# Performance work log

Measured on AMD Instinct MI355X. Metric: run time of the kernel, lower is better.

Reference implementation:

```python
import jax, jax.numpy as jnp
import numpy as np

N, E = 32768, 8192            # num_nodes, num_hyperedges
ND, ED, HD, OD, NH = 128, 128, 64, 128, 4  # node/edge/hidden/output dims, heads
EPS = 1e-8


def min_max_normalize(x):
    # per-feature (column-wise) min-max normalization, as in utils.min_max_normalize_cuda
    mn = x.min(axis=0)
    mx = x.max(axis=0)
    return (x - mn) / (mx - mn + EPS)


def setup_inputs() -> dict:
    key = jax.random.key(0)
    ks = jax.random.split(key, 12)
    s = 0.05
    node_features = jax.random.normal(ks[0], (N, ND), jnp.float32)
    # sparse-ish binary incidence matrix stored dense (as the torch code uses dense mm)
    incidence_matrix = (jax.random.uniform(ks[1], (N, E)) < 0.01).astype(jnp.float32)
    edge_features = jax.random.normal(ks[2], (E, ED), jnp.float32)
    # stacked per-head parameters (heads are chained, so head input dim == ND == OD)
    nodeW = jax.random.normal(ks[3], (NH, ND, HD), jnp.float32) * s
    nodeB = jnp.zeros((NH, HD), jnp.float32)
    edgeW = jax.random.normal(ks[4], (NH, ED, HD), jnp.float32) * s
    edgeB = jnp.zeros((NH, HD), jnp.float32)
    attnW = jax.random.normal(ks[5], (NH, HD, 1), jnp.float32) * s
    attnB = jnp.zeros((NH, 1), jnp.float32)
    outW = jax.random.normal(ks[6], (NH, HD, OD), jnp.float32) * s
    outB = jnp.zeros((NH, OD), jnp.float32)
    return dict(node_features=node_features, incidence_matrix=incidence_matrix,
                edge_features=edge_features, nodeW=nodeW, nodeB=nodeB,
                edgeW=edgeW, edgeB=edgeB, attnW=attnW, attnB=attnB,
                outW=outW, outB=outB)


def reference(node_features, incidence_matrix, edge_features,
              nodeW, nodeB, edgeW, edgeB, attnW, attnB, outW, outB):
    # node degree normalizer, shared across heads
    deg = incidence_matrix.sum(axis=1, keepdims=True) + EPS  # [N, 1]
    x = node_features
    for h in range(NH):  # heads are applied sequentially (chained), per original forward
        tn = x @ nodeW[h] + nodeB[h]                       # [N, HD]
        te = edge_features @ edgeW[h] + edgeB[h]           # [E, HD]
        agg = (incidence_matrix @ te) / deg                # [N, HD] mean over incident edges
        scores = (tn + agg) @ attnW[h] + attnB[h]          # [N, 1]
        scores = jnp.where(scores >= 0, scores, 0.2 * scores)  # LeakyReLU(0.2)
        coeffs = jax.nn.sigmoid(scores)                    # [N, 1]
        upd = coeffs * agg + tn                            # gated residual
        upd = upd @ outW[h] + outB[h]                      # [N, OD]
        upd = min_max_normalize(upd)
        x = jax.nn.relu(upd)                               # ReLU applied after each head
    # dropout is identity at inference; output_transform is defined but never used
    return x
```

## Files before the change

### kernel.cpp

```cpp
#include <hip/hip_runtime.h>
#include <cstdint>
#include <cstddef>

#define N_NODES 32768
#define N_EDGES 8192
#define ND 128
#define HD 64
#define OD 128
#define NH 4
#define EPSV 1e-8f
#define NBLOCKS 256
#define ROWS 128
#define LDW 132

__device__ __forceinline__ unsigned encf(float f) {
  unsigned b = __float_as_uint(f);
  return (b & 0x80000000u) ? ~b : (b | 0x80000000u);
}
__device__ __forceinline__ float decf(unsigned u) {
  unsigned b = (u & 0x80000000u) ? (u & 0x7fffffffu) : ~u;
  return __uint_as_float(b);
}
__device__ __forceinline__ unsigned aload(const unsigned* p) {
  return __hip_atomic_load(p, __ATOMIC_RELAXED, __HIP_MEMORY_SCOPE_AGENT);
}

__device__ __forceinline__ void gsync(unsigned* cnt, unsigned* gen) {
  __syncthreads();
  if (threadIdx.x == 0) {
    __threadfence();
    const unsigned g = __hip_atomic_load(gen, __ATOMIC_ACQUIRE, __HIP_MEMORY_SCOPE_AGENT);
    if (__hip_atomic_fetch_add(cnt, 1u, __ATOMIC_ACQ_REL, __HIP_MEMORY_SCOPE_AGENT) == NBLOCKS - 1u) {
      __hip_atomic_store(cnt, 0u, __ATOMIC_RELAXED, __HIP_MEMORY_SCOPE_AGENT);
      __hip_atomic_store(gen, g + 1u, __ATOMIC_RELEASE, __HIP_MEMORY_SCOPE_AGENT);
    } else {
      while (__hip_atomic_load(gen, __ATOMIC_ACQUIRE, __HIP_MEMORY_SCOPE_AGENT) == g) {
        __builtin_amdgcn_s_sleep(2);
      }
    }
    __threadfence();
  }
  __syncthreads();
}

__global__ __launch_bounds__(512, 2) void k_fused(
    const float* __restrict__ nf, const float* __restrict__ inc,
    const float* __restrict__ ef,
    const float* __restrict__ nodeW, const float* __restrict__ nodeB,
    const float* __restrict__ edgeW, const float* __restrict__ edgeB,
    const float* __restrict__ attnW, const float* __restrict__ attnB,
    const float* __restrict__ outW, const float* __restrict__ outB,
    unsigned* __restrict__ fin_mn, unsigned* __restrict__ fin_mx,
    unsigned* __restrict__ bar_cnt, unsigned* __restrict__ bar_gen,
    float* __restrict__ outp)
{
  __shared__ __align__(16) float xs[ROWS * LDW];
  __shared__ __align__(16) float ps[ROWS * LDW];
  __shared__ float s_deg[ROWS];
  __shared__ int s_idx[2][512];
  __shared__ int s_cnt[2];
  __shared__ float s_red[4 * 128];
  __shared__ float s_mm[8 * 128];

  const int t = threadIdx.x;
  const int r0 = blockIdx.x * ROWS;

  #pragma unroll
  for (int i = 0; i < 8; i++) {
    const int f = t + i * 512;
    const int row = f >> 5;
    const int c4 = (f & 31) * 4;
    *(float4*)&xs[row * LDW + c4] = *(const float4*)(nf + (size_t)(r0 + row) * ND + c4);
  }

  const int dim = t & 127;
  const int sub = t >> 7;
  float4 vreg[4];
  {
    const float* irow = inc + (size_t)r0 * N_EDGES;
    #pragma unroll
    for (int i = 0; i < 4; i++) vreg[i] = *(const float4*)(irow + (t + i * 512) * 4);
  }
  #pragma unroll 1
  for (int row = 0; row < ROWS; row++) {
    const int buf = row & 1;
    if (t == 0) s_cnt[buf] = 0;
    __syncthreads();
    #pragma unroll
    for (int i = 0; i < 4; i++) {
      const int c = (t + i * 512) * 4;
      const float4 v = vreg[i];
      if (v.x != 0.f) s_idx[buf][atomicAdd(&s_cnt[buf], 1)] = c;
      if (v.y != 0.f) s_idx[buf][atomicAdd(&s_cnt[buf], 1)] = c + 1;
      if (v.z != 0.f) s_idx[buf][atomicAdd(&s_cnt[buf], 1)] = c + 2;
      if (v.w != 0.f) s_idx[buf][atomicAdd(&s_cnt[buf], 1)] = c + 3;
    }
    if (row + 1 < ROWS) {
      const float* irow = inc + (size_t)(r0 + row + 1) * N_EDGES;
      #pragma unroll
      for (int i = 0; i < 4; i++) vreg[i] = *(const float4*)(irow + (t + i * 512) * 4);
    }
    __syncthreads();
    const int cnt = min(s_cnt[buf], 512);
    float acc = 0.f;
    int i = sub;
    for (; i + 28 < cnt; i += 32) {
      float sv = 0.f;
      #pragma unroll
      for (int u2 = 0; u2 < 8; u2++) sv += ef[(size_t)s_idx[buf][i + u2 * 4] * ND + dim];
      acc += sv;
    }
    for (; i + 12 < cnt; i += 16) {
      float sv = 0.f;
      #pragma unroll
      for (int u2 = 0; u2 < 4; u2++) sv += ef[(size_t)s_idx[buf][i + u2 * 4] * ND + dim];
      acc += sv;
    }
    for (; i < cnt; i += 4) acc += ef[(size_t)s_idx[buf][i] * ND + dim];
    s_red[sub * 128 + dim] = acc;
    __syncthreads();
    if (t < 128) {
      ps[row * LDW + t] = s_red[t] + s_red[128 + t] + s_red[256 + t] + s_red[384 + t];
      if (t == 0) s_deg[row] = (float)cnt;
    }
  }
  __syncthreads();

  const int lane = t & 63;
  const int wv = t >> 6;
  const int o = lane & 7;
  const int rA = (wv << 4) + (lane >> 3);
  const int rB = rA + 8;
  const int j0 = o * 8;
  const int obase = lane & 56;

  #pragma unroll 1
  for (int h = 0; h < NH; h++) {
    const float* nW = nodeW + (size_t)h * ND * HD;
    const float* eW = edgeW + (size_t)h * ND * HD;
    const float* oW = outW + (size_t)h * HD * OD;
    const float* nB = nodeB + (size_t)h * HD;
    const float* eB = edgeB + (size_t)h * HD;
    const float* aW = attnW + (size_t)h * HD;
    const float  aB = attnB[h];

    if (h > 0) {
      const unsigned* pmn = fin_mn + (size_t)(h - 1) * 128;
      const unsigned* pmx = fin_mx + (size_t)(h - 1) * 128;
      if (t < 128) s_red[t] = decf(aload(&pmn[t]));
      else if (t < 256) s_red[t] = decf(aload(&pmx[t - 128]));
      __syncthreads();
      const int rr = t >> 2;
      const int c0 = (t & 3) * 32;
      #pragma unroll
      for (int i = 0; i < 32; i++) {
        const float mnv = s_red[c0 + i];
        const float mxv = s_red[128 + c0 + i];
        const float v = (xs[rr * LDW + c0 + i] - mnv) / (mxv - mnv + EPSV);
        xs[rr * LDW + c0 + i] = v > 0.f ? v : 0.f;
      }
      __syncthreads();
    }

    float tnA[8], tnB[8], agA[8], agB[8];
    #pragma unroll
    for (int j = 0; j < 8; j++) { tnA[j] = 0.f; tnB[j] = 0.f; agA[j] = 0.f; agB[j] = 0.f; }
    for (int k4 = 0; k4 < ND; k4 += 4) {
      const float4 xa = *(const float4*)&xs[rA * LDW + k4];
      const float4 xb = *(const float4*)&xs[rB * LDW + k4];
      const float4 pa = *(const float4*)&ps[rA * LDW + k4];
      const float4 pb = *(const float4*)&ps[rB * LDW + k4];
      const float xav[4] = {xa.x, xa.y, xa.z, xa.w};
      const float xbv[4] = {xb.x, xb.y, xb.z, xb.w};
      const float pav[4] = {pa.x, pa.y, pa.z, pa.w};
      const float pbv[4] = {pb.x, pb.y, pb.z, pb.w};
      #pragma unroll
      for (int kk = 0; kk < 4; kk++) {
        const int k = k4 + kk;
        const float4 n0 = *(const float4*)(nW + (size_t)k * HD + j0);
        const float4 n1 = *(const float4*)(nW + (size_t)k * HD + j0 + 4);
        const float4 e0 = *(const float4*)(eW + (size_t)k * HD + j0);
        const float4 e1 = *(const float4*)(eW + (size_t)k * HD + j0 + 4);
        const float nn[8] = {n0.x, n0.y, n0.z, n0.w, n1.x, n1.y, n1.z, n1.w};
        const float ee[8] = {e0.x, e0.y, e0.z, e0.w, e1.x, e1.y, e1.z, e1.w};
        #pragma unroll
        for (int j = 0; j < 8; j++) {
          tnA[j] = fmaf(xav[kk], nn[j], tnA[j]);
          tnB[j] = fmaf(xbv[kk], nn[j], tnB[j]);
          agA[j] = fmaf(pav[kk], ee[j], agA[j]);
          agB[j] = fmaf(pbv[kk], ee[j], agB[j]);
        }
      }
    }

    const float rsA = s_deg[rA], rsB = s_deg[rB];
    const float dA = rsA + EPSV, dB = rsB + EPSV;
    const float iA = 1.f / dA, iB = 1.f / dB;
    float spA = 0.f, spB = 0.f;
    #pragma unroll
    for (int j = 0; j < 8; j++) {
      const float nb = nB[j0 + j], eb = eB[j0 + j], aw = aW[j0 + j];
      const float tA = tnA[j] + nb, tB = tnB[j] + nb;
      const float aA = fmaf(rsA, eb, agA[j]) * iA;
      const float aB = fmaf(rsB, eb, agB[j]) * iB;
      tnA[j] = tA; tnB[j] = tB; agA[j] = aA; agB[j] = aB;
      spA = fmaf(tA + aA, aw, spA);
      spB = fmaf(tB + aB, aw, spB);
    }
    spA += __shfl_xor(spA, 1); spA += __shfl_xor(spA, 2); spA += __shfl_xor(spA, 4);
    spB += __shfl_xor(spB, 1); spB += __shfl_xor(spB, 2); spB += __shfl_xor(spB, 4);
    float sA = spA + aB, sB = spB + aB;
    sA = (sA >= 0.f) ? sA : 0.2f * sA;
    sB = (sB >= 0.f) ? sB : 0.2f * sB;
    const float cA = 1.f / (1.f + expf(-sA));
    const float cB = 1.f / (1.f + expf(-sB));
    float uA[8], uB[8];
    #pragma unroll
    for (int j = 0; j < 8; j++) {
      uA[j] = fmaf(cA, agA[j], tnA[j]);
      uB[j] = fmaf(cB, agB[j], tnB[j]);
    }

    const int oc0 = o * 16;
    float ya[16], yb[16];
    #pragma unroll
    for (int i4 = 0; i4 < 4; i4++) {
      const float4 bv = *(const float4*)(outB + (size_t)h * OD + oc0 + i4 * 4);
      ya[i4 * 4 + 0] = bv.x; ya[i4 * 4 + 1] = bv.y; ya[i4 * 4 + 2] = bv.z; ya[i4 * 4 + 3] = bv.w;
      yb[i4 * 4 + 0] = bv.x; yb[i4 * 4 + 1] = bv.y; yb[i4 * 4 + 2] = bv.z; yb[i4 * 4 + 3] = bv.w;
    }
    #pragma unroll 8
    for (int k = 0; k < HD; k++) {
      const float ukA = __shfl(uA[k & 7], obase + (k >> 3));
      const float ukB = __shfl(uB[k & 7], obase + (k >> 3));
      #pragma unroll
      for (int i4 = 0; i4 < 4; i4++) {
        const float4 ov = *(const float4*)(oW + (size_t)k * OD + oc0 + i4 * 4);
        const float oo[4] = {ov.x, ov.y, ov.z, ov.w};
        #pragma unroll
        for (int c = 0; c < 4; c++) {
          ya[i4 * 4 + c] = fmaf(ukA, oo[c], ya[i4 * 4 + c]);
          yb[i4 * 4 + c] = fmaf(ukB, oo[c], yb[i4 * 4 + c]);
        }
      }
    }

    __syncthreads();
    #pragma unroll
    for (int i4 = 0; i4 < 4; i4++) {
      *(float4*)&xs[rA * LDW + oc0 + i4 * 4] =
          make_float4(ya[i4 * 4 + 0], ya[i4 * 4 + 1], ya[i4 * 4 + 2], ya[i4 * 4 + 3]);
      *(float4*)&xs[rB * LDW + oc0 + i4 * 4] =
          make_float4(yb[i4 * 4 + 0], yb[i4 * 4 + 1], yb[i4 * 4 + 2], yb[i4 * 4 + 3]);
    }
    __syncthreads();
    {
      const int col = t & 127;
      const int s4 = t >> 7;
      float lo = 3.4e38f, hi = -3.4e38f;
      for (int r = s4; r < ROWS; r += 4) {
        const float v = xs[r * LDW + col];
        lo = fminf(lo, v); hi = fmaxf(hi, v);
      }
      s_mm[s4 * 128 + col] = lo;
      s_mm[512 + s4 * 128 + col] = hi;
      __syncthreads();
      if (t < 128) {
        const float l = fminf(fminf(s_mm[t], s_mm[128 + t]), fminf(s_mm[256 + t], s_mm[384 + t]));
        const float hh = fmaxf(fmaxf(s_mm[512 + t], s_mm[640 + t]), fmaxf(s_mm[768 + t], s_mm[896 + t]));
        atomicMin(&fin_mn[(size_t)h * 128 + t], encf(l));
        atomicMax(&fin_mx[(size_t)h * 128 + t], encf(hh));
      }
    }
    gsync(bar_cnt, bar_gen);
  }

  if (t < 128) s_red[t] = decf(aload(&fin_mn[3 * 128 + t]));
  else if (t < 256) s_red[t] = decf(aload(&fin_mx[3 * 128 + (t - 128)]));
  __syncthreads();
  #pragma unroll
  for (int i = 0; i < 8; i++) {
    const int f = t + i * 512;
    const int row = f >> 5;
    const int c4 = (f & 31) * 4;
    const float4 v = *(const float4*)&xs[row * LDW + c4];
    float va[4] = {v.x, v.y, v.z, v.w};
    #pragma unroll
    for (int c = 0; c < 4; c++) {
      const float mnv = s_red[c4 + c];
      const float mxv = s_red[128 + c4 + c];
      const float nv = (va[c] - mnv) / (mxv - mnv + EPSV);
      va[c] = nv > 0.f ? nv : 0.f;
    }
    *(float4*)(outp + (size_t)(r0 + row) * OD + c4) = make_float4(va[0], va[1], va[2], va[3]);
  }
}

extern "C" void kernel_launch(void* const* d_in, const int* in_sizes, int n_in,
                              void* d_out, int out_size, void* d_ws, size_t ws_size,
                              hipStream_t stream)
{
  const float* node_features = (const float*)d_in[0];
  const float* incidence     = (const float*)d_in[1];
  const float* edge_features = (const float*)d_in[2];
  const float* nodeW = (const float*)d_in[3];
  const float* nodeB = (const float*)d_in[4];
  const float* edgeW = (const float*)d_in[5];
  const float* edgeB = (const float*)d_in[6];
  const float* attnW = (const float*)d_in[7];
  const float* attnB = (const float*)d_in[8];
  const float* outW  = (const float*)d_in[9];
  const float* outB  = (const float*)d_in[10];
  float* out = (float*)d_out;

  unsigned* fin_mn = (unsigned*)d_ws;
  unsigned* fin_mx = fin_mn + NH * 128;
  unsigned* bar    = fin_mx + NH * 128;

  hipMemsetAsync(fin_mn, 0xFF, NH * 128 * sizeof(unsigned), stream);
  hipMemsetAsync(fin_mx, 0x00, NH * 128 * sizeof(unsigned), stream);
  hipMemsetAsync(bar, 0x00, 2 * sizeof(unsigned), stream);

  k_fused<<<NBLOCKS, 512, 0, stream>>>(
      node_features, incidence, edge_features,
      nodeW, nodeB, edgeW, edgeB, attnW, attnB, outW, outB,
      fin_mn, fin_mx, bar, bar + 1, out);
}
```

Measured before the change: 1.974 ms.

## Give each wavefront its own incidence rows with ballot-based compaction and nontemporal loads

Replaces the block-wide, row-by-row incidence scan with a per-wavefront scheme in which each of the 8 waves owns 16 rows. Nonzero column indices are compacted with ballot/mbcnt into a wave-private LDS list, and the edge-feature gather uses float2 per lane. The incidence matrix is streamed with software-pipelined nontemporal loads. This removes the per-row __syncthreads barriers, shared-memory atomics and cross-sub-group reduction that dominated the 1 GB incidence streaming phase. Per-row index capacity drops to 256 entries, which is well above the expected count of about 82.

```diff
diff --git a/kernel.cpp b/kernel.cpp
--- a/kernel.cpp
+++ b/kernel.cpp
@@ -12,6 +12,9 @@
 #define NBLOCKS 256
 #define ROWS 128
 #define LDW 132
+#define WCAP 256
+
+typedef float vf4 __attribute__((ext_vector_type(4)));
 
 __device__ __forceinline__ unsigned encf(float f) {
   unsigned b = __float_as_uint(f);
@@ -57,13 +60,14 @@
   __shared__ __align__(16) float xs[ROWS * LDW];
   __shared__ __align__(16) float ps[ROWS * LDW];
   __shared__ float s_deg[ROWS];
-  __shared__ int s_idx[2][512];
-  __shared__ int s_cnt[2];
+  __shared__ int s_widx[8 * WCAP];
   __shared__ float s_red[4 * 128];
   __shared__ float s_mm[8 * 128];
 
   const int t = threadIdx.x;
   const int r0 = blockIdx.x * ROWS;
+  const int lane = t & 63;
+  const int wv = t >> 6;
 
   #pragma unroll
   for (int i = 0; i < 8; i++) {
@@ -73,61 +77,82 @@
     *(float4*)&xs[row * LDW + c4] = *(const float4*)(nf + (size_t)(r0 + row) * ND + c4);
   }
 
-  const int dim = t & 127;
-  const int sub = t >> 7;
-  float4 vreg[4];
   {
-    const float* irow = inc + (size_t)r0 * N_EDGES;
-    #pragma unroll
-    for (int i = 0; i < 4; i++) vreg[i] = *(const float4*)(irow + (t + i * 512) * 4);
-  }
-  #pragma unroll 1
-  for (int row = 0; row < ROWS; row++) {
-    const int buf = row & 1;
-    if (t == 0) s_cnt[buf] = 0;
-    __syncthreads();
-    #pragma unroll
-    for (int i = 0; i < 4; i++) {
-      const int c = (t + i * 512) * 4;
-      const float4 v = vreg[i];
-      if (v.x != 0.f) s_idx[buf][atomicAdd(&s_cnt[buf], 1)] = c;
-      if (v.y != 0.f) s_idx[buf][atomicAdd(&s_cnt[buf], 1)] = c + 1;
-      if (v.z != 0.f) s_idx[buf][atomicAdd(&s_cnt[buf], 1)] = c + 2;
-      if (v.w != 0.f) s_idx[buf][atomicAdd(&s_cnt[buf], 1)] = c + 3;
-    }
-    if (row + 1 < ROWS) {
-      const float* irow = inc + (size_t)(r0 + row + 1) * N_EDGES;
-      #pragma unroll
-      for (int i = 0; i < 4; i++) vreg[i] = *(const float4*)(irow + (t + i * 512) * 4);
-    }
-    __syncthreads();
-    const int cnt = min(s_cnt[buf], 512);
-    float acc = 0.f;
-    int i = sub;
-    for (; i + 28 < cnt; i += 32) {
-      float sv = 0.f;
-      #pragma unroll
-      for (int u2 = 0; u2 < 8; u2++) sv += ef[(size_t)s_idx[buf][i + u2 * 4] * ND + dim];
-      acc += sv;
-    }
-    for (; i + 12 < cnt; i += 16) {
-      float sv = 0.f;
-      #pragma unroll
-      for (int u2 = 0; u2 < 4; u2++) sv += ef[(size_t)s_idx[buf][i + u2 * 4] * ND + dim];
-      acc += sv;
-    }
-    for (; i < cnt; i += 4) acc += ef[(size_t)s_idx[buf][i] * ND + dim];
-    s_red[sub * 128 + dim] = acc;
-    __syncthreads();
-    if (t < 128) {
-      ps[row * LDW + t] = s_red[t] + s_red[128 + t] + s_red[256 + t] + s_red[384 + t];
-      if (t == 0) s_deg[row] = (float)cnt;
+    const int wrow0 = wv * 16;
+    const int wvb = wv * WCAP;
+    unsigned cnt = 0;
+    auto compact = [&](const vf4* w, int ebase) {
+      #pragma unroll
+      for (int i = 0; i < 8; i++) {
+        #pragma unroll
+        for (int c = 0; c < 4; c++) {
+          const bool nz = (w[i][c] != 0.f);
+          const unsigned long long m = __ballot(nz);
+          if (m) {
+            const unsigned lt = __builtin_amdgcn_mbcnt_hi(
+                (unsigned)(m >> 32), __builtin_amdgcn_mbcnt_lo((unsigned)m, 0u));
+            const unsigned pos = cnt + lt;
+            if (nz && pos < WCAP) s_widx[wvb + pos] = ebase + i * 256 + lane * 4 + c;
+            cnt += (unsigned)__popcll(m);
+          }
+        }
+      }
+    };
+    vf4 A[8], B[8];
+    {
+      const float* rp0 = inc + (size_t)(r0 + wrow0) * N_EDGES;
+      #pragma unroll
+      for (int i = 0; i < 8; i++)
+        A[i] = __builtin_nontemporal_load((const vf4*)(rp0 + i * 256 + lane * 4));
+    }
+    #pragma unroll 1
+    for (int rr = 0; rr < 16; rr++) {
+      const int row = wrow0 + rr;
+      const float* rp = inc + (size_t)(r0 + row) * N_EDGES;
+      cnt = 0;
+      #pragma unroll
+      for (int i = 0; i < 8; i++)
+        B[i] = __builtin_nontemporal_load((const vf4*)(rp + 2048 + i * 256 + lane * 4));
+      compact(A, 0);
+      #pragma unroll
+      for (int i = 0; i < 8; i++)
+        A[i] = __builtin_nontemporal_load((const vf4*)(rp + 4096 + i * 256 + lane * 4));
+      compact(B, 2048);
+      #pragma unroll
+      for (int i = 0; i < 8; i++)
+        B[i] = __builtin_nontemporal_load((const vf4*)(rp + 6144 + i * 256 + lane * 4));
+      compact(A, 4096);
+      if (rr + 1 < 16) {
+        const float* rpn = rp + N_EDGES;
+        #pragma unroll
+        for (int i = 0; i < 8; i++)
+          A[i] = __builtin_nontemporal_load((const vf4*)(rpn + i * 256 + lane * 4));
+      }
+      compact(B, 6144);
+      const unsigned g = cnt < WCAP ? cnt : WCAP;
+      float ax = 0.f, ay = 0.f;
+      unsigned i = 0;
+      for (; i + 8 <= g; i += 8) {
+        float2 vv[8];
+        #pragma unroll
+        for (int u = 0; u < 8; u++) {
+          const int e = s_widx[wvb + i + u];
+          vv[u] = *(const float2*)(ef + (size_t)e * ND + (lane << 1));
+        }
+        #pragma unroll
+        for (int u = 0; u < 8; u++) { ax += vv[u].x; ay += vv[u].y; }
+      }
+      for (; i < g; i++) {
+        const int e = s_widx[wvb + i];
+        const float2 v = *(const float2*)(ef + (size_t)e * ND + (lane << 1));
+        ax += v.x; ay += v.y;
+      }
+      *(float2*)&ps[row * LDW + (lane << 1)] = make_float2(ax, ay);
+      if (lane == 0) s_deg[row] = (float)cnt;
     }
   }
   __syncthreads();
 
-  const int lane = t & 63;
-  const int wv = t >> 6;
   const int o = lane & 7;
   const int rA = (wv << 4) + (lane >> 3);
   const int rB = rA + 8;
```

Result: faster. 1.805 ms (-8.6%).
